# Kernel tuning notes

Hardware: AMD Instinct MI355X
Metric: run time of the kernel (lower is better)

Reference implementation:

```python
import jax, jax.numpy as jnp
import numpy as np

B, N, KD, VD, ID, H = 2, 2048, 1024, 1024, 1024, 16
HD = ID // H
SCALE = ID ** (-0.5)  # module quirk: scale uses inner_dim, not head_dim
EPS = 1e-5


def layernorm(x, g, b):
    mu = jnp.mean(x, axis=-1, keepdims=True)
    var = jnp.var(x, axis=-1, keepdims=True)
    return (x - mu) * jax.lax.rsqrt(var + EPS) * g + b


def setup_inputs() -> dict:
    key = jax.random.key(0)
    ks = jax.random.split(key, 12)
    d = {
        "keys": jax.random.normal(ks[0], (B, N, KD), jnp.float32),
        "values": jax.random.normal(ks[1], (B, N, VD), jnp.float32),
        "qk_norm_g": jnp.ones((KD,), jnp.float32),
        "qk_norm_b": jnp.zeros((KD,), jnp.float32),
        "value_norm_g": jnp.ones((VD,), jnp.float32),
        "value_norm_b": jnp.zeros((VD,), jnp.float32),
        "key_norm_g": jnp.ones((ID,), jnp.float32),
        "key_norm_b": jnp.zeros((ID,), jnp.float32),
        "query_norm_g": jnp.ones((ID,), jnp.float32),
        "query_norm_b": jnp.zeros((ID,), jnp.float32),
        "w_qk": jax.random.normal(ks[2], (KD, 2 * ID), jnp.float32) * (KD ** -0.5),
        "w_v": jax.random.normal(ks[3], (VD, ID), jnp.float32) * (VD ** -0.5),
        "w_out": jax.random.normal(ks[4], (ID, VD), jnp.float32) * (ID ** -0.5),
        "b_out": jnp.zeros((VD,), jnp.float32),
    }
    return d


def reference(keys, values, qk_norm_g, qk_norm_b, value_norm_g, value_norm_b,
              key_norm_g, key_norm_b, query_norm_g, query_norm_b,
              w_qk, w_v, w_out, b_out):
    keys = layernorm(keys, qk_norm_g, qk_norm_b)
    values = layernorm(values, value_norm_g, value_norm_b)
    qk = keys @ w_qk  # [B,N,2*ID]
    q, k = qk[..., :ID], qk[..., ID:]
    q = layernorm(q, query_norm_g, query_norm_b)
    k = layernorm(k, key_norm_g, key_norm_b)
    # b n (h d) -> b h n d
    q = q.reshape(B, N, H, HD).transpose(0, 2, 1, 3)
    k = k.reshape(B, N, H, HD).transpose(0, 2, 1, 3)
    v = (values @ w_v).reshape(B, N, H, HD).transpose(0, 2, 1, 3)
    dots = jnp.einsum('bhqd,bhkd->bhqk', q, k) * SCALE
    attn = jax.nn.softmax(dots, axis=-1)
    out = jnp.einsum('bhqk,bhkd->bhqd', attn, v)
    out = out.transpose(0, 2, 1, 3).reshape(B, N, ID)
    return out @ w_out + b_out
```

## Files before the change

kernel.cpp:

```cpp
#include <hip/hip_runtime.h>
#include <hip/hip_bf16.h>
#include <type_traits>


typedef __hip_bfloat16 bf16;
typedef __attribute__((ext_vector_type(8))) short bf16x8;
typedef __attribute__((ext_vector_type(4))) float f32x4;

#define MFMA_BF16(a, b, c) __builtin_amdgcn_mfma_f32_16x16x32_bf16((a), (b), (c), 0, 0, 0)

__device__ __forceinline__ float us2f(unsigned short u) {
  unsigned int v = ((unsigned int)u) << 16;
  return __builtin_bit_cast(float, v);
}

__device__ __forceinline__ unsigned pack_bf16x2(float a, float b) {
  union { __hip_bfloat162 h; unsigned u; } cv;
  cv.h = __float22bfloat162_rn(float2{a, b});
  return cv.u;
}

__device__ __forceinline__ unsigned pack_bf16x2_trunc(float a, float b) {
  return __builtin_amdgcn_perm(__builtin_bit_cast(unsigned, b),
                               __builtin_bit_cast(unsigned, a), 0x07060302u);
}

__device__ __forceinline__ void gl_lds16(const bf16* g, bf16* l) {
  __builtin_amdgcn_global_load_lds(
      (const __attribute__((address_space(1))) void*)g,
      (__attribute__((address_space(3))) void*)l, 16, 0, 0);
}

template <typename TIN>
__global__ __launch_bounds__(256) void ln2_kernel(
    const TIN* __restrict__ in0, const TIN* __restrict__ in1, int stride,
    const float* __restrict__ g0, const float* __restrict__ b0,
    const float* __restrict__ g1, const float* __restrict__ b1,
    bf16* __restrict__ out0, bf16* __restrict__ out1, int D,
    float sc0, float sc1)
{
  const int which = blockIdx.y;
  const TIN* in = which ? in1 : in0;
  const float* gamma = which ? g1 : g0;
  const float* beta = which ? b1 : b0;
  bf16* out = which ? out1 : out0;
  const float sc = which ? sc1 : sc0;
  const int row = blockIdx.x;
  const int t = threadIdx.x;
  float x0, x1, x2, x3;
  if constexpr (std::is_same_v<TIN, float>) {
    float4 u = *(const float4*)(in + (size_t)row * stride + t * 4);
    x0 = u.x; x1 = u.y; x2 = u.z; x3 = u.w;
  } else {
    ushort4 u = *(const ushort4*)(in + (size_t)row * stride + t * 4);
    x0 = us2f(u.x); x1 = us2f(u.y); x2 = us2f(u.z); x3 = us2f(u.w);
  }
  float s = x0 + x1 + x2 + x3;
  float s2 = x0 * x0 + x1 * x1 + x2 * x2 + x3 * x3;
#pragma unroll
  for (int m = 1; m < 64; m <<= 1) {
    s += __shfl_xor(s, m);
    s2 += __shfl_xor(s2, m);
  }
  __shared__ float red[10];
  const int w = t >> 6, lane = t & 63;
  if (lane == 0) { red[w] = s; red[4 + w] = s2; }
  __syncthreads();
  if (t == 0) {
    float S = red[0] + red[1] + red[2] + red[3];
    float S2 = red[4] + red[5] + red[6] + red[7];
    float mu = S / (float)D;
    float var = S2 / (float)D - mu * mu;
    red[8] = mu;
    red[9] = rsqrtf(var + 1e-5f);
  }
  __syncthreads();
  const float mu = red[8], rs = red[9];
  float4 g4 = *(const float4*)(gamma + t * 4);
  float4 b4 = *(const float4*)(beta + t * 4);
  uint2 o;
  o.x = pack_bf16x2(((x0 - mu) * rs * g4.x + b4.x) * sc, ((x1 - mu) * rs * g4.y + b4.y) * sc);
  o.y = pack_bf16x2(((x2 - mu) * rs * g4.z + b4.z) * sc, ((x3 - mu) * rs * g4.w + b4.w) * sc);
  *(uint2*)(out + (size_t)row * D + t * 4) = o;
}

__global__ __launch_bounds__(256) void transpose3_kernel(
    const float* __restrict__ s0, bf16* __restrict__ d0,
    const float* __restrict__ s1, bf16* __restrict__ d1,
    const float* __restrict__ s2, bf16* __restrict__ d2)
{
  const int z = blockIdx.z;
  if (z > 0 && blockIdx.x >= 16) return;
  const float* in = (z == 0) ? s0 : (z == 1) ? s1 : s2;
  bf16* out = (z == 0) ? d0 : (z == 1) ? d1 : d2;
  const int R = 1024, C = (z == 0) ? 2048 : 1024;
  __shared__ float tile[64][68];
  const int r0 = blockIdx.y * 64, c0 = blockIdx.x * 64;
  const int t = threadIdx.x;
  const int lr = t >> 2, lc = (t & 3) * 16;
  const float* src = in + (size_t)(r0 + lr) * C + (c0 + lc);
#pragma unroll
  for (int i = 0; i < 4; ++i) {
    float4 u = *(const float4*)(src + i * 4);
    tile[lr][lc + i * 4 + 0] = u.x;
    tile[lr][lc + i * 4 + 1] = u.y;
    tile[lr][lc + i * 4 + 2] = u.z;
    tile[lr][lc + i * 4 + 3] = u.w;
  }
  __syncthreads();
  __align__(16) bf16 tmp[16];
#pragma unroll
  for (int j = 0; j < 16; ++j) tmp[j] = __float2bfloat16(tile[lc + j][lr]);
  bf16* dst = out + (size_t)(c0 + lr) * R + (r0 + lc);
  *(bf16x8*)dst       = *(const bf16x8*)&tmp[0];
  *(bf16x8*)(dst + 8) = *(const bf16x8*)&tmp[8];
}

template <int BM, int BN, int TMODE, typename TOUT>
__global__ __launch_bounds__(256) void gemm_bt_kernel(
    const bf16* __restrict__ A, const bf16* __restrict__ Bt,
    const float* __restrict__ bias, TOUT* __restrict__ C,
    int M, int N, int K, int has_bias)
{
  constexpr int MT = BM / 32, NT = BN / 32;
  constexpr int ASL = BM / 32, BSL = BN / 32;
  constexpr int BUFE = (BM + BN) * 64;
  __shared__ __align__(16) bf16 smem[2 * BUFE];
  const int t = threadIdx.x;
  const int w = t >> 6, lane = t & 63, l15 = lane & 15, quad = lane >> 4;
  const int wy = w >> 1, wx = w & 1;
  const bf16* Ab = A + (size_t)blockIdx.y * BM * K;
  const bf16* Bb = Bt + (size_t)blockIdx.x * BN * K;
  f32x4 acc[MT][NT] = {};

  const bf16* aptr[ASL];
  const bf16* bptr[BSL];
#pragma unroll
  for (int i = 0; i < ASL; ++i) {
    int s = i * 256 + t, row = s >> 3, c = (s & 7) ^ (row & 7);
    aptr[i] = Ab + (size_t)row * K + (c << 3);
  }
#pragma unroll
  for (int i = 0; i < BSL; ++i) {
    int s = i * 256 + t, row = s >> 3, c = (s & 7) ^ (row & 7);
    bptr[i] = Bb + (size_t)row * K + (c << 3);
  }

  auto stage = [&](bf16* buf, int kc) {
#pragma unroll
    for (int i = 0; i < ASL; ++i)
      gl_lds16(aptr[i] + kc, buf + (i * 256 + t) * 8);
#pragma unroll
    for (int i = 0; i < BSL; ++i)
      gl_lds16(bptr[i] + kc, buf + BM * 64 + (i * 256 + t) * 8);
  };

  const int sw = (quad ^ (l15 & 7)) << 3;
  const int NK = K >> 6;

  stage(smem, 0);

  for (int kt = 0; kt < NK; ++kt) {
    const int cur = kt & 1;
    bf16* lA = smem + cur * BUFE;
    bf16* lB = lA + BM * 64;
    __builtin_amdgcn_s_barrier();
    if (kt + 1 < NK) {
      stage(smem + (cur ^ 1) * BUFE, (kt + 1) << 6);
      asm volatile("s_waitcnt vmcnt(8)" ::: "memory");
    } else {
      asm volatile("s_waitcnt vmcnt(0)" ::: "memory");
    }
    __builtin_amdgcn_s_barrier();

#pragma unroll
    for (int h = 0; h < 2; ++h) {
      const int so = sw ^ (h << 5);
      bf16x8 af[MT], bfr[NT];
#pragma unroll
      for (int mt = 0; mt < MT; ++mt)
        af[mt] = *(const bf16x8*)&lA[(wy * (BM / 2) + mt * 16 + l15) * 64 + so];
#pragma unroll
      for (int nt = 0; nt < NT; ++nt)
        bfr[nt] = *(const bf16x8*)&lB[(wx * (BN / 2) + nt * 16 + l15) * 64 + so];
#pragma unroll
      for (int mt = 0; mt < MT; ++mt)
#pragma unroll
        for (int nt = 0; nt < NT; ++nt)
          acc[mt][nt] = MFMA_BF16(af[mt], bfr[nt], acc[mt][nt]);
    }
  }

  if constexpr (TMODE == 1) {
    constexpr int STR = BM + 8;
    bf16* lOut = smem;
    __syncthreads();
#pragma unroll
    for (int mt = 0; mt < MT; ++mt)
#pragma unroll
      for (int nt = 0; nt < NT; ++nt) {
        const int d = wx * (BN / 2) + nt * 16 + l15;
        const int n = wy * (BM / 2) + mt * 16 + quad * 4;
        uint2 pk;
        pk.x = pack_bf16x2(acc[mt][nt][0], acc[mt][nt][1]);
        pk.y = pack_bf16x2(acc[mt][nt][2], acc[mt][nt][3]);
        *(uint2*)&lOut[d * STR + n] = pk;
      }
    __syncthreads();
    const int row0 = blockIdx.y * BM;
    const int bidx = row0 >> 11, n0 = row0 & 2047;
    const int col0 = blockIdx.x * BN;
    const int d = t >> 1, half = (t & 1) * (BM / 2);
    const bf16* srcp = &lOut[d * STR + half];
    bf16* g = (bf16*)C + ((size_t)(bidx << 10) + col0 + d) * 2048 + n0 + half;
#pragma unroll
    for (int j = 0; j < BM / 16; ++j)
      *(bf16x8*)(g + j * 8) = *(const bf16x8*)(srcp + j * 8);
  } else {
    const int row_base = blockIdx.y * BM + wy * (BM / 2);
    const int col_base = blockIdx.x * BN + wx * (BN / 2);
#pragma unroll
    for (int mt = 0; mt < MT; ++mt)
#pragma unroll
      for (int nt = 0; nt < NT; ++nt) {
        const int col = col_base + nt * 16 + l15;
        const float bb = has_bias ? bias[col] : 0.0f;
#pragma unroll
        for (int r = 0; r < 4; ++r) {
          const int row = row_base + mt * 16 + quad * 4 + r;
          float v = acc[mt][nt][r] + bb;
          if constexpr (std::is_same_v<TOUT, bf16>)
            C[(size_t)row * N + col] = __float2bfloat16(v);
          else
            C[(size_t)row * N + col] = v;
        }
      }
  }
}

__global__ __launch_bounds__(256) void flash_kernel(
    const bf16* __restrict__ Q, const bf16* __restrict__ Km,
    const bf16* __restrict__ Vt, bf16* __restrict__ O)
{
  __shared__ __align__(16) bf16 smem[9216 + 8192 + 8192 + 8192];
  bf16* lP = smem;
  bf16* lQ = smem + 9216;
  bf16* lKb = smem + 9216 + 8192;
  bf16* lVb = smem + 9216 + 8192 + 8192;
  const int t = threadIdx.x;
  const int w = t >> 6, lane = t & 63, l15 = lane & 15, quad = lane >> 4;
  const int qt = blockIdx.x, bh = blockIdx.y;
  const int b = bh >> 4, h = bh & 15;
  const int qrow0 = b * 2048 + qt * 128;
  const bf16* qbase = Q + (size_t)qrow0 * 1024 + h * 64;
  const bf16* kbase = Km + ((size_t)(b * 2048)) * 1024 + h * 64;
  const bf16* vbase = Vt + ((size_t)(b * 1024 + h * 64)) * 2048;
  bf16* lPm = lP + w * (32 * 72);

  const int sr0 = t >> 3, sc0 = ((t & 7) ^ (sr0 & 7)) << 3;
  const int sr1 = (256 + t) >> 3, sc1 = (((256 + t) & 7) ^ (sr1 & 7)) << 3;
  const bf16* kp0 = kbase + sr0 * 1024 + sc0;
  const bf16* kp1 = kbase + sr1 * 1024 + sc1;
  const bf16* vp0 = vbase + sr0 * 2048 + sc0;
  const bf16* vp1 = vbase + sr1 * 2048 + sc1;

#pragma unroll
  for (int i = 0; i < 4; ++i) {
    int s = i * 256 + t;
    int row = s >> 3, c = (s & 7) ^ (row & 7);
    gl_lds16(qbase + (size_t)row * 1024 + (c << 3), lQ + s * 8);
  }
  gl_lds16(kp0, lKb + t * 8);
  gl_lds16(kp1, lKb + (256 + t) * 8);
  gl_lds16(vp0, lVb + t * 8);
  gl_lds16(vp1, lVb + (256 + t) * 8);
  asm volatile("s_waitcnt vmcnt(4)" ::: "memory");
  __builtin_amdgcn_s_barrier();

  const int sw = (quad ^ (l15 & 7)) << 3;
  bf16x8 qf[2][2];
#pragma unroll
  for (int mset = 0; mset < 2; ++mset) {
    const int row = w * 32 + mset * 16 + l15;
    qf[mset][0] = *(const bf16x8*)&lQ[row * 64 + sw];
    qf[mset][1] = *(const bf16x8*)&lQ[row * 64 + (sw ^ 32)];
  }

  f32x4 o_acc[4][2] = {};
  f32x4 l_vec[2] = {};

  for (int kt = 0; kt < 32; ++kt) {
    const int cur = kt & 1;
    bf16* lK = lKb + cur * 4096;
    bf16* lV = lVb + cur * 4096;
    bf16* lKn = lKb + (cur ^ 1) * 4096;
    bf16* lVn = lVb + (cur ^ 1) * 4096;

    __builtin_amdgcn_s_barrier();
    {
      const int ktn = (kt + 1) & 31;
      const int ko = ktn << 16;
      const int vo = ktn << 6;
      gl_lds16(kp0 + ko, lKn + t * 8);
      gl_lds16(kp1 + ko, lKn + (256 + t) * 8);
      gl_lds16(vp0 + vo, lVn + t * 8);
      gl_lds16(vp1 + vo, lVn + (256 + t) * 8);
    }
    asm volatile("s_waitcnt vmcnt(4)" ::: "memory");
    __builtin_amdgcn_s_barrier();

    bf16x8 kf[4][2];
#pragma unroll
    for (int nt = 0; nt < 4; ++nt) {
      kf[nt][0] = *(const bf16x8*)&lK[(nt * 16 + l15) * 64 + sw];
      kf[nt][1] = *(const bf16x8*)&lK[(nt * 16 + l15) * 64 + (sw ^ 32)];
    }

#pragma unroll
    for (int mset = 0; mset < 2; ++mset) {
#pragma unroll
      for (int nt = 0; nt < 4; ++nt) {
        f32x4 z = {};
        z = MFMA_BF16(kf[nt][0], qf[mset][0], z);
        z = MFMA_BF16(kf[nt][1], qf[mset][1], z);
        f32x4 p;
#pragma unroll
        for (int r = 0; r < 4; ++r) p[r] = __builtin_amdgcn_exp2f(z[r]);
        l_vec[mset] += p;
        uint2 pk;
        pk.x = pack_bf16x2_trunc(p[0], p[1]);
        pk.y = pack_bf16x2_trunc(p[2], p[3]);
        *(uint2*)&lPm[(mset * 16 + l15) * 72 + nt * 16 + quad * 4] = pk;
      }
    }

    bf16x8 vf[4][2];
#pragma unroll
    for (int dt = 0; dt < 4; ++dt) {
      vf[dt][0] = *(const bf16x8*)&lV[(dt * 16 + l15) * 64 + sw];
      vf[dt][1] = *(const bf16x8*)&lV[(dt * 16 + l15) * 64 + (sw ^ 32)];
    }
    asm volatile("s_waitcnt lgkmcnt(0)" ::: "memory");

#pragma unroll
    for (int mset = 0; mset < 2; ++mset) {
      const bf16* pr = &lPm[(mset * 16 + l15) * 72 + quad * 8];
      bf16x8 pf0 = *(const bf16x8*)pr;
      bf16x8 pf1 = *(const bf16x8*)(pr + 32);
#pragma unroll
      for (int dt = 0; dt < 4; ++dt) {
        o_acc[dt][mset] = MFMA_BF16(vf[dt][0], pf0, o_acc[dt][mset]);
        o_acc[dt][mset] = MFMA_BF16(vf[dt][1], pf1, o_acc[dt][mset]);
      }
    }
  }

#pragma unroll
  for (int mset = 0; mset < 2; ++mset) {
    float tsum = l_vec[mset][0] + l_vec[mset][1] + l_vec[mset][2] + l_vec[mset][3];
    tsum += __shfl_xor(tsum, 16);
    tsum += __shfl_xor(tsum, 32);
    const float inv = 1.0f / tsum;
    const int m = qrow0 + w * 32 + mset * 16 + l15;
#pragma unroll
    for (int dt = 0; dt < 4; ++dt) {
      uint2 ok;
      ok.x = pack_bf16x2(o_acc[dt][mset][0] * inv, o_acc[dt][mset][1] * inv);
      ok.y = pack_bf16x2(o_acc[dt][mset][2] * inv, o_acc[dt][mset][3] * inv);
      *(uint2*)&O[(size_t)m * 1024 + h * 64 + dt * 16 + quad * 4] = ok;
    }
  }
}

extern "C" void kernel_launch(void* const* d_in, const int* in_sizes, int n_in,
                              void* d_out, int out_size, void* d_ws, size_t ws_size,
                              hipStream_t stream)
{
  (void)in_sizes; (void)n_in; (void)out_size; (void)ws_size;
  const float* keys   = (const float*)d_in[0];
  const float* values = (const float*)d_in[1];
  const float* qk_g   = (const float*)d_in[2];
  const float* qk_b   = (const float*)d_in[3];
  const float* val_g  = (const float*)d_in[4];
  const float* val_b  = (const float*)d_in[5];
  const float* key_g  = (const float*)d_in[6];
  const float* key_b  = (const float*)d_in[7];
  const float* qry_g  = (const float*)d_in[8];
  const float* qry_b  = (const float*)d_in[9];
  const float* w_qk   = (const float*)d_in[10];
  const float* w_v    = (const float*)d_in[11];
  const float* w_out  = (const float*)d_in[12];
  const float* b_out  = (const float*)d_in[13];
  float* out = (float*)d_out;

  const float CEXP = 0.03125f * 1.44269504f;

  char* ws = (char*)d_ws;
  const size_t MB = 1024 * 1024;
  bf16* keys_ln   = (bf16*)(ws + 0);
  bf16* values_ln = (bf16*)(ws + 8 * MB);
  bf16* qk        = (bf16*)(ws + 16 * MB);
  bf16* attn      = (bf16*)(ws + 16 * MB);
  bf16* vt        = (bf16*)(ws + 24 * MB);
  bf16* qln       = (bf16*)(ws + 32 * MB);
  bf16* kln       = (bf16*)(ws + 40 * MB);
  bf16* wqkT      = (bf16*)(ws + 48 * MB);
  bf16* wvT       = (bf16*)(ws + 52 * MB);
  bf16* woutT     = (bf16*)(ws + 54 * MB);

  ln2_kernel<float><<<dim3(4096, 2), 256, 0, stream>>>(
      keys, values, 1024, qk_g, qk_b, val_g, val_b, keys_ln, values_ln, 1024, 1.0f, 1.0f);
  transpose3_kernel<<<dim3(32, 16, 3), 256, 0, stream>>>(w_qk, wqkT, w_v, wvT, w_out, woutT);
  gemm_bt_kernel<128, 128, 0, bf16><<<dim3(16, 32), 256, 0, stream>>>(keys_ln, wqkT, nullptr, qk, 4096, 2048, 1024, 0);
  ln2_kernel<bf16><<<dim3(4096, 2), 256, 0, stream>>>(
      qk, qk + 1024, 2048, qry_g, qry_b, key_g, key_b, qln, kln, 1024, CEXP, 1.0f);
  gemm_bt_kernel<128, 128, 1, bf16><<<dim3(8, 32), 256, 0, stream>>>(values_ln, wvT, nullptr, vt, 4096, 1024, 1024, 0);
  flash_kernel<<<dim3(16, 32), 256, 0, stream>>>(qln, kln, vt, attn);
  gemm_bt_kernel<128, 128, 0, float><<<dim3(8, 32), 256, 0, stream>>>(attn, woutT, b_out, out, 4096, 1024, 1024, 1);
}
```

Baseline: 240.7 us.

## Keep softmax probabilities in registers and shrink GEMM tiles for more blocks

The flash kernel no longer round-trips P through LDS. It permutes the K rows it loads so that the S accumulator layout matches the B-operand layout of the PV MFMA, packs exp values directly into bf16x8 registers, and raises wave priority around the PV MFMAs. This removes the P scratch buffer, its LDS writes and reads, and a waitcnt. Separately, the V-projection and output GEMMs switch from 128x128 to 128x64 tiles, doubling the grid to 512 blocks for better CU occupancy, with waitcnt counts and the transpose epilogue adjusted to match.

```diff
diff --git a/kernel.cpp b/kernel.cpp
--- a/kernel.cpp
+++ b/kernel.cpp
@@ -167,7 +167,10 @@
     __builtin_amdgcn_s_barrier();
     if (kt + 1 < NK) {
       stage(smem + (cur ^ 1) * BUFE, (kt + 1) << 6);
-      asm volatile("s_waitcnt vmcnt(8)" ::: "memory");
+      if constexpr (ASL + BSL == 8)
+        asm volatile("s_waitcnt vmcnt(8)" ::: "memory");
+      else
+        asm volatile("s_waitcnt vmcnt(6)" ::: "memory");
     } else {
       asm volatile("s_waitcnt vmcnt(0)" ::: "memory");
     }
@@ -192,7 +195,9 @@
   }
 
   if constexpr (TMODE == 1) {
+    static_assert(BM * BN == 8192, "TMODE1 epilogue assumes 8192 els/block");
     constexpr int STR = BM + 8;
+    static_assert(BN * STR <= 2 * BUFE, "lOut must fit staging buffers");
     bf16* lOut = smem;
     __syncthreads();
 #pragma unroll
@@ -210,11 +215,12 @@
     const int row0 = blockIdx.y * BM;
     const int bidx = row0 >> 11, n0 = row0 & 2047;
     const int col0 = blockIdx.x * BN;
-    const int d = t >> 1, half = (t & 1) * (BM / 2);
-    const bf16* srcp = &lOut[d * STR + half];
-    bf16* g = (bf16*)C + ((size_t)(bidx << 10) + col0 + d) * 2048 + n0 + half;
-#pragma unroll
-    for (int j = 0; j < BM / 16; ++j)
+    constexpr int CPR = BM / 32;
+    const int d = t / CPR, off = (t % CPR) * 32;
+    const bf16* srcp = &lOut[d * STR + off];
+    bf16* g = (bf16*)C + ((size_t)(bidx << 10) + col0 + d) * 2048 + n0 + off;
+#pragma unroll
+    for (int j = 0; j < 4; ++j)
       *(bf16x8*)(g + j * 8) = *(const bf16x8*)(srcp + j * 8);
   } else {
     const int row_base = blockIdx.y * BM + wy * (BM / 2);
@@ -242,11 +248,10 @@
     const bf16* __restrict__ Q, const bf16* __restrict__ Km,
     const bf16* __restrict__ Vt, bf16* __restrict__ O)
 {
-  __shared__ __align__(16) bf16 smem[9216 + 8192 + 8192 + 8192];
-  bf16* lP = smem;
-  bf16* lQ = smem + 9216;
-  bf16* lKb = smem + 9216 + 8192;
-  bf16* lVb = smem + 9216 + 8192 + 8192;
+  __shared__ __align__(16) bf16 smem[8192 + 8192 + 8192];
+  bf16* lQ = smem;
+  bf16* lKb = smem + 8192;
+  bf16* lVb = smem + 16384;
   const int t = threadIdx.x;
   const int w = t >> 6, lane = t & 63, l15 = lane & 15, quad = lane >> 4;
   const int qt = blockIdx.x, bh = blockIdx.y;
@@ -255,12 +260,13 @@
   const bf16* qbase = Q + (size_t)qrow0 * 1024 + h * 64;
   const bf16* kbase = Km + ((size_t)(b * 2048)) * 1024 + h * 64;
   const bf16* vbase = Vt + ((size_t)(b * 1024 + h * 64)) * 2048;
-  bf16* lPm = lP + w * (32 * 72);
 
   const int sr0 = t >> 3, sc0 = ((t & 7) ^ (sr0 & 7)) << 3;
   const int sr1 = (256 + t) >> 3, sc1 = (((256 + t) & 7) ^ (sr1 & 7)) << 3;
-  const bf16* kp0 = kbase + sr0 * 1024 + sc0;
-  const bf16* kp1 = kbase + sr1 * 1024 + sc1;
+  const int gr0 = (sr0 & 0x23) | ((sr0 & 0x0C) << 1) | ((sr0 & 0x10) >> 2);
+  const int gr1 = (sr1 & 0x23) | ((sr1 & 0x0C) << 1) | ((sr1 & 0x10) >> 2);
+  const bf16* kp0 = kbase + gr0 * 1024 + sc0;
+  const bf16* kp1 = kbase + gr1 * 1024 + sc1;
   const bf16* vp0 = vbase + sr0 * 2048 + sc0;
   const bf16* vp1 = vbase + sr1 * 2048 + sc1;
 
@@ -316,21 +322,29 @@
       kf[nt][1] = *(const bf16x8*)&lK[(nt * 16 + l15) * 64 + (sw ^ 32)];
     }
 
+    bf16x8 pa[2][2];
 #pragma unroll
     for (int mset = 0; mset < 2; ++mset) {
 #pragma unroll
-      for (int nt = 0; nt < 4; ++nt) {
-        f32x4 z = {};
-        z = MFMA_BF16(kf[nt][0], qf[mset][0], z);
-        z = MFMA_BF16(kf[nt][1], qf[mset][1], z);
-        f32x4 p;
-#pragma unroll
-        for (int r = 0; r < 4; ++r) p[r] = __builtin_amdgcn_exp2f(z[r]);
-        l_vec[mset] += p;
-        uint2 pk;
-        pk.x = pack_bf16x2_trunc(p[0], p[1]);
-        pk.y = pack_bf16x2_trunc(p[2], p[3]);
-        *(uint2*)&lPm[(mset * 16 + l15) * 72 + nt * 16 + quad * 4] = pk;
+      for (int half = 0; half < 2; ++half) {
+        f32x4 z0 = {}, z1 = {};
+        z0 = MFMA_BF16(kf[2 * half + 0][0], qf[mset][0], z0);
+        z0 = MFMA_BF16(kf[2 * half + 0][1], qf[mset][1], z0);
+        z1 = MFMA_BF16(kf[2 * half + 1][0], qf[mset][0], z1);
+        z1 = MFMA_BF16(kf[2 * half + 1][1], qf[mset][1], z1);
+        f32x4 p0, p1;
+#pragma unroll
+        for (int r = 0; r < 4; ++r) {
+          p0[r] = __builtin_amdgcn_exp2f(z0[r]);
+          p1[r] = __builtin_amdgcn_exp2f(z1[r]);
+        }
+        l_vec[mset] += p0 + p1;
+        union { unsigned u[4]; bf16x8 v; } cv;
+        cv.u[0] = pack_bf16x2_trunc(p0[0], p0[1]);
+        cv.u[1] = pack_bf16x2_trunc(p0[2], p0[3]);
+        cv.u[2] = pack_bf16x2_trunc(p1[0], p1[1]);
+        cv.u[3] = pack_bf16x2_trunc(p1[2], p1[3]);
+        pa[mset][half] = cv.v;
       }
     }
 
@@ -340,19 +354,16 @@
       vf[dt][0] = *(const bf16x8*)&lV[(dt * 16 + l15) * 64 + sw];
       vf[dt][1] = *(const bf16x8*)&lV[(dt * 16 + l15) * 64 + (sw ^ 32)];
     }
-    asm volatile("s_waitcnt lgkmcnt(0)" ::: "memory");
-
-#pragma unroll
-    for (int mset = 0; mset < 2; ++mset) {
-      const bf16* pr = &lPm[(mset * 16 + l15) * 72 + quad * 8];
-      bf16x8 pf0 = *(const bf16x8*)pr;
-      bf16x8 pf1 = *(const bf16x8*)(pr + 32);
+
+    __builtin_amdgcn_s_setprio(1);
+#pragma unroll
+    for (int mset = 0; mset < 2; ++mset)
 #pragma unroll
       for (int dt = 0; dt < 4; ++dt) {
-        o_acc[dt][mset] = MFMA_BF16(vf[dt][0], pf0, o_acc[dt][mset]);
-        o_acc[dt][mset] = MFMA_BF16(vf[dt][1], pf1, o_acc[dt][mset]);
+        o_acc[dt][mset] = MFMA_BF16(vf[dt][0], pa[mset][0], o_acc[dt][mset]);
+        o_acc[dt][mset] = MFMA_BF16(vf[dt][1], pa[mset][1], o_acc[dt][mset]);
       }
-    }
+    __builtin_amdgcn_s_setprio(0);
   }
 
 #pragma unroll
@@ -414,7 +425,7 @@
   gemm_bt_kernel<128, 128, 0, bf16><<<dim3(16, 32), 256, 0, stream>>>(keys_ln, wqkT, nullptr, qk, 4096, 2048, 1024, 0);
   ln2_kernel<bf16><<<dim3(4096, 2), 256, 0, stream>>>(
       qk, qk + 1024, 2048, qry_g, qry_b, key_g, key_b, qln, kln, 1024, CEXP, 1.0f);
-  gemm_bt_kernel<128, 128, 1, bf16><<<dim3(8, 32), 256, 0, stream>>>(values_ln, wvT, nullptr, vt, 4096, 1024, 1024, 0);
+  gemm_bt_kernel<128, 64, 1, bf16><<<dim3(16, 32), 256, 0, stream>>>(values_ln, wvT, nullptr, vt, 4096, 1024, 1024, 0);
   flash_kernel<<<dim3(16, 32), 256, 0, stream>>>(qln, kln, vt, attn);
-  gemm_bt_kernel<128, 128, 0, float><<<dim3(8, 32), 256, 0, stream>>>(attn, woutT, b_out, out, 4096, 1024, 1024, 1);
-}
+  gemm_bt_kernel<128, 64, 0, float><<<dim3(16, 32), 256, 0, stream>>>(attn, woutT, b_out, out, 4096, 1024, 1024, 1);
+}
```

Result: faster. 223.0 us (-7.3%).
